# Performance work log

Hardware: AMD Instinct MI355X
Metric: run time of the kernel (lower is better)

Reference implementation:

```python
import jax, jax.numpy as jnp
import numpy as np

B, N = 16, 131072
C_MID, C_OUT = 128, 16


def setup_inputs() -> dict:
    key = jax.random.key(0)
    k1, k2, k3, k4 = jax.random.split(key, 4)
    # points in roughly [-0.5, 0.5] so cube indexing covers the grids
    x = jax.random.uniform(k1, (B, N, 3), dtype=jnp.float32) - 0.5
    W1 = jax.random.normal(k2, (C_MID, 3), dtype=jnp.float32) * 0.1
    b1 = jnp.zeros((C_MID,), jnp.float32)
    W2 = jax.random.normal(k3, (C_OUT, C_MID), dtype=jnp.float32) * 0.1
    b2 = jnp.zeros((C_OUT,), jnp.float32)
    # fixed per-batch permutations (deterministic stand-in for torch.randperm)
    perm = jnp.stack([jax.random.permutation(jax.random.fold_in(k4, i), N)
                      for i in range(B)]).astype(jnp.int32)
    return {"x": x, "W1": W1, "b1": b1, "W2": W2, "b2": b2, "perm": perm}


def point_to_cell(pts, feat, W, H, D):
    # pts float [B,N,3] already clamped to [0, dim-1]; cast like torch LongTensor
    idx = pts.astype(jnp.int32)
    flat = (idx[..., 0] * H + idx[..., 1]) * D + idx[..., 2]  # [B,N]
    Bb, Nn, C = feat.shape

    def scatter_one(fi, fe):
        grid = jnp.zeros((W * H * D, C), feat.dtype)
        return grid.at[fi].set(fe)

    cell = jax.vmap(scatter_one)(flat, feat)           # [B, WHD, C]
    return cell.transpose(0, 2, 1).reshape(Bb, C, W, H, D)


def reference(x, W1, b1, W2, b2, perm):
    # PointNetfeatLocal: 1x1 Conv1d stack == per-point MLP 3 -> 128 -> 16
    h = jnp.maximum(jnp.einsum('bnc,hc->bnh', x, W1) + b1, 0.0)
    feat = jnp.einsum('bnh,oh->bno', h, W2) + b2       # [B,N,16]
    # shuffle_points_feat: per-batch permutation gather
    xs = jnp.take_along_axis(x, perm[..., None], axis=1)
    fs = jnp.take_along_axis(feat, perm[..., None], axis=1)
    # batch_grid_pooling32 / 64
    cube32 = jnp.clip(xs * 32.0 + 16.5, 0.0, 31.0)
    cube64 = jnp.clip(xs * 64.0 + 32.5, 0.0, 63.0)
    feat_cell32 = point_to_cell(cube32, fs, 32, 32, 32)  # [B,16,32,32,32]
    feat_cell64 = point_to_cell(cube64, fs, 64, 64, 64)  # [B,16,64,64,64]
    return feat_cell32, feat_cell64
```

## Files before the change

### kernel.cpp

```cpp
#include <hip/hip_runtime.h>

namespace {
constexpr int kB = 16;
constexpr int kN = 131072;
constexpr int kNLog = 17;
constexpr int kCMid = 128;
constexpr int kCOut = 16;
constexpr int kCells32Log = 15;
constexpr int kCells64Log = 18;
constexpr int kCells32 = 1 << kCells32Log;
constexpr int kCells64 = 1 << kCells64Log;
constexpr long kOut32Elems = (long)kB * kCOut * kCells32;
constexpr int kP = 4;
}

__global__ __launch_bounds__(256) void pack_weights(
    const float* __restrict__ W1, const float* __restrict__ b1,
    const float* __restrict__ W2,
    float* __restrict__ W1p, float* __restrict__ W2t)
{
    const int t = threadIdx.x;
    for (int k = t; k < kCMid; k += 256) {
        W1p[k * 4 + 0] = W1[k * 3 + 0];
        W1p[k * 4 + 1] = W1[k * 3 + 1];
        W1p[k * 4 + 2] = W1[k * 3 + 2];
        W1p[k * 4 + 3] = b1[k];
    }
    for (int idx = t; idx < kCOut * kCMid; idx += 256) {
        const int c = idx >> 7;
        const int k = idx & 127;
        W2t[k * kCOut + c] = W2[idx];
    }
}

__global__ __launch_bounds__(256) void fused_mlp_scatter(
    const float* __restrict__ x,
    const int* __restrict__ perm,
    const float* __restrict__ W1p, const float* __restrict__ W2t,
    const float* __restrict__ b2,
    unsigned int* __restrict__ win32, unsigned int* __restrict__ win64,
    float* __restrict__ feat)
{
    const int t = threadIdx.x;
    const long base = (long)blockIdx.x * (256 * kP);

    float x0[kP], x1[kP], x2[kP];

    #pragma unroll
    for (int p = 0; p < kP; ++p) {
        const long gid = base + p * 256 + t;
        const int b = (int)(gid >> kNLog);
        const int i = (int)(gid & (kN - 1));
        const int j = perm[gid];
        const float* xp = x + ((long)b * kN + j) * 3;
        const float v0 = xp[0], v1 = xp[1], v2 = xp[2];
        x0[p] = v0; x1[p] = v1; x2[p] = v2;

        const int ix32 = (int)fminf(fmaxf(__fadd_rn(__fmul_rn(v0, 32.0f), 16.5f), 0.0f), 31.0f);
        const int iy32 = (int)fminf(fmaxf(__fadd_rn(__fmul_rn(v1, 32.0f), 16.5f), 0.0f), 31.0f);
        const int iz32 = (int)fminf(fmaxf(__fadd_rn(__fmul_rn(v2, 32.0f), 16.5f), 0.0f), 31.0f);
        const int ix64 = (int)fminf(fmaxf(__fadd_rn(__fmul_rn(v0, 64.0f), 32.5f), 0.0f), 63.0f);
        const int iy64 = (int)fminf(fmaxf(__fadd_rn(__fmul_rn(v1, 64.0f), 32.5f), 0.0f), 63.0f);
        const int iz64 = (int)fminf(fmaxf(__fadd_rn(__fmul_rn(v2, 64.0f), 32.5f), 0.0f), 63.0f);
        const unsigned int pri = (unsigned int)(i + 1);
        atomicMax(&win32[b * kCells32 + (ix32 * 32 + iy32) * 32 + iz32], pri);
        atomicMax(&win64[b * kCells64 + (ix64 * 64 + iy64) * 64 + iz64], pri);
    }

    float acc[kP][kCOut];
    #pragma unroll
    for (int p = 0; p < kP; ++p)
        #pragma unroll
        for (int c = 0; c < kCOut; ++c) acc[p][c] = 0.0f;

    const float4* __restrict__ w1v = (const float4*)W1p;
    const float4* __restrict__ w2v = (const float4*)W2t;

    #pragma unroll 4
    for (int k = 0; k < kCMid; ++k) {
        const float4 w1 = w1v[k];
        float h[kP];
        #pragma unroll
        for (int p = 0; p < kP; ++p)
            h[p] = fmaxf(fmaf(w1.x, x0[p], fmaf(w1.y, x1[p], fmaf(w1.z, x2[p], w1.w))), 0.0f);
        #pragma unroll
        for (int q = 0; q < 4; ++q) {
            const float4 w = w2v[k * 4 + q];
            #pragma unroll
            for (int p = 0; p < kP; ++p) {
                acc[p][4 * q + 0] = fmaf(w.x, h[p], acc[p][4 * q + 0]);
                acc[p][4 * q + 1] = fmaf(w.y, h[p], acc[p][4 * q + 1]);
                acc[p][4 * q + 2] = fmaf(w.z, h[p], acc[p][4 * q + 2]);
                acc[p][4 * q + 3] = fmaf(w.w, h[p], acc[p][4 * q + 3]);
            }
        }
    }

    const float4 bq0 = ((const float4*)b2)[0];
    const float4 bq1 = ((const float4*)b2)[1];
    const float4 bq2 = ((const float4*)b2)[2];
    const float4 bq3 = ((const float4*)b2)[3];

    #pragma unroll
    for (int p = 0; p < kP; ++p) {
        const long gid = base + p * 256 + t;
        float4* fp = (float4*)(feat + gid * kCOut);
        fp[0] = make_float4(acc[p][0]  + bq0.x, acc[p][1]  + bq0.y, acc[p][2]  + bq0.z, acc[p][3]  + bq0.w);
        fp[1] = make_float4(acc[p][4]  + bq1.x, acc[p][5]  + bq1.y, acc[p][6]  + bq1.z, acc[p][7]  + bq1.w);
        fp[2] = make_float4(acc[p][8]  + bq2.x, acc[p][9]  + bq2.y, acc[p][10] + bq2.z, acc[p][11] + bq2.w);
        fp[3] = make_float4(acc[p][12] + bq3.x, acc[p][13] + bq3.y, acc[p][14] + bq3.z, acc[p][15] + bq3.w);
    }
}

template <int CLOG, bool RECOMPUTE>
__global__ __launch_bounds__(256) void gather_cells(
    const unsigned int* __restrict__ win,
    const float* __restrict__ feat,
    const int* __restrict__ perm,
    const float* __restrict__ x,
    const float* __restrict__ W1p, const float* __restrict__ W2t,
    const float* __restrict__ b2,
    float* __restrict__ out)
{
    constexpr int cells = 1 << CLOG;
    const long gid = (long)blockIdx.x * 256 + threadIdx.x;
    const int b = (int)(gid >> CLOG);
    const int cell = (int)(gid & (cells - 1));
    const unsigned int w = win[gid];

    float v[kCOut];
    if (w == 0u) {
        #pragma unroll
        for (int c = 0; c < kCOut; ++c) v[c] = 0.0f;
    } else if (!RECOMPUTE) {
        const int i = (int)(w - 1u);
        const float4* fp = (const float4*)(feat + (((long)b << kNLog) + i) * kCOut);
        const float4 f0 = fp[0], f1 = fp[1], f2 = fp[2], f3 = fp[3];
        v[0] = f0.x; v[1] = f0.y; v[2]  = f0.z; v[3]  = f0.w;
        v[4] = f1.x; v[5] = f1.y; v[6]  = f1.z; v[7]  = f1.w;
        v[8] = f2.x; v[9] = f2.y; v[10] = f2.z; v[11] = f2.w;
        v[12] = f3.x; v[13] = f3.y; v[14] = f3.z; v[15] = f3.w;
    } else {
        const int i = (int)(w - 1u);
        const int j = perm[((long)b << kNLog) + i];
        const float* xp = x + ((long)b * kN + j) * 3;
        const float v0 = xp[0], v1 = xp[1], v2 = xp[2];
        #pragma unroll
        for (int c = 0; c < kCOut; ++c) v[c] = 0.0f;
        #pragma unroll 4
        for (int k = 0; k < kCMid; ++k) {
            const float4 w1 = ((const float4*)W1p)[k];
            const float h = fmaxf(fmaf(w1.x, v0, fmaf(w1.y, v1, fmaf(w1.z, v2, w1.w))), 0.0f);
            #pragma unroll
            for (int q = 0; q < 4; ++q) {
                const float4 wq = ((const float4*)W2t)[k * 4 + q];
                v[4 * q + 0] = fmaf(wq.x, h, v[4 * q + 0]);
                v[4 * q + 1] = fmaf(wq.y, h, v[4 * q + 1]);
                v[4 * q + 2] = fmaf(wq.z, h, v[4 * q + 2]);
                v[4 * q + 3] = fmaf(wq.w, h, v[4 * q + 3]);
            }
        }
        #pragma unroll
        for (int c = 0; c < kCOut; ++c) v[c] += b2[c];
    }

    float* op = out + (((long)b * kCOut) << CLOG) + cell;
    #pragma unroll
    for (int c = 0; c < kCOut; ++c) op[(long)c << CLOG] = v[c];
}

extern "C" void kernel_launch(void* const* d_in, const int* in_sizes, int n_in,
                              void* d_out, int out_size, void* d_ws, size_t ws_size,
                              hipStream_t stream)
{
    const float* x  = (const float*)d_in[0];
    const float* W1 = (const float*)d_in[1];
    const float* b1 = (const float*)d_in[2];
    const float* W2 = (const float*)d_in[3];
    const float* b2 = (const float*)d_in[4];
    const int* perm = (const int*)d_in[5];

    float* out32 = (float*)d_out;
    float* out64 = out32 + kOut32Elems;

    float* W1p = (float*)d_ws;
    float* W2t = W1p + kCMid * 4;
    unsigned int* win32 = (unsigned int*)((char*)d_ws + 16384);
    unsigned int* win64 = win32 + (size_t)kB * kCells32;
    const size_t winnerBytes = (size_t)kB * (kCells32 + kCells64) * sizeof(unsigned int);
    float* feat = (float*)((char*)win32 + winnerBytes);
    const size_t featBytes = (size_t)kB * kN * kCOut * sizeof(float);
    const bool storeFeat = ws_size >= 16384 + winnerBytes + featBytes;

    hipMemsetAsync(win32, 0, winnerBytes, stream);
    pack_weights<<<1, 256, 0, stream>>>(W1, b1, W2, W1p, W2t);

    const int nPtsBlocks = (int)(((long)kB * kN) / (256 * kP));
    const int n32Blocks  = (int)(((long)kB * kCells32) / 256);
    const int n64Blocks  = (int)(((long)kB * kCells64) / 256);
    dim3 blk(256);

    fused_mlp_scatter<<<nPtsBlocks, blk, 0, stream>>>(
        x, perm, W1p, W2t, b2, win32, win64, feat);

    if (storeFeat) {
        gather_cells<kCells32Log, false><<<n32Blocks, blk, 0, stream>>>(
            win32, feat, perm, x, W1p, W2t, b2, out32);
        gather_cells<kCells64Log, false><<<n64Blocks, blk, 0, stream>>>(
            win64, feat, perm, x, W1p, W2t, b2, out64);
    } else {
        gather_cells<kCells32Log, true><<<n32Blocks, blk, 0, stream>>>(
            win32, feat, perm, x, W1p, W2t, b2, out32);
        gather_cells<kCells64Log, true><<<n64Blocks, blk, 0, stream>>>(
            win64, feat, perm, x, W1p, W2t, b2, out64);
    }
}
```

Baseline: 320.6 us.

## Compute MLP only for winning points inside gather instead of materialising features

Drops the MLP from the scatter kernel, which now only records per-cell winning point indices. The gather kernels always recompute the 3→128→16 MLP for each occupied cell's winner, so the feature buffer is no longer written for all 2M points and read back. This removes the large feature write and gather read traffic and the MLP work for points that never win a cell. In exchange, occupied cells in both grids recompute the MLP, and points that win a cell in both grids are computed twice. Launch bounds of 4 blocks per SM are also added.

```diff
diff --git a/kernel.cpp b/kernel.cpp
--- a/kernel.cpp
+++ b/kernel.cpp
@@ -11,7 +11,6 @@
 constexpr int kCells32 = 1 << kCells32Log;
 constexpr int kCells64 = 1 << kCells64Log;
 constexpr long kOut32Elems = (long)kB * kCOut * kCells32;
-constexpr int kP = 4;
 }
 
 __global__ __launch_bounds__(256) void pack_weights(
@@ -33,89 +32,34 @@
     }
 }
 
-__global__ __launch_bounds__(256) void fused_mlp_scatter(
+__global__ __launch_bounds__(256, 4) void scatter_winners(
     const float* __restrict__ x,
     const int* __restrict__ perm,
-    const float* __restrict__ W1p, const float* __restrict__ W2t,
-    const float* __restrict__ b2,
-    unsigned int* __restrict__ win32, unsigned int* __restrict__ win64,
-    float* __restrict__ feat)
+    unsigned int* __restrict__ win32, unsigned int* __restrict__ win64)
 {
-    const int t = threadIdx.x;
-    const long base = (long)blockIdx.x * (256 * kP);
+    const long gid = (long)blockIdx.x * 256 + threadIdx.x;
+    const int b = (int)(gid >> kNLog);
+    const int i = (int)(gid & (kN - 1));
+    const int j = perm[gid];
 
-    float x0[kP], x1[kP], x2[kP];
+    const float* xp = x + ((long)b * kN + j) * 3;
+    const float v0 = xp[0], v1 = xp[1], v2 = xp[2];
 
-    #pragma unroll
-    for (int p = 0; p < kP; ++p) {
-        const long gid = base + p * 256 + t;
-        const int b = (int)(gid >> kNLog);
-        const int i = (int)(gid & (kN - 1));
-        const int j = perm[gid];
-        const float* xp = x + ((long)b * kN + j) * 3;
-        const float v0 = xp[0], v1 = xp[1], v2 = xp[2];
-        x0[p] = v0; x1[p] = v1; x2[p] = v2;
+    const int ix32 = (int)fminf(fmaxf(__fadd_rn(__fmul_rn(v0, 32.0f), 16.5f), 0.0f), 31.0f);
+    const int iy32 = (int)fminf(fmaxf(__fadd_rn(__fmul_rn(v1, 32.0f), 16.5f), 0.0f), 31.0f);
+    const int iz32 = (int)fminf(fmaxf(__fadd_rn(__fmul_rn(v2, 32.0f), 16.5f), 0.0f), 31.0f);
+    const int ix64 = (int)fminf(fmaxf(__fadd_rn(__fmul_rn(v0, 64.0f), 32.5f), 0.0f), 63.0f);
+    const int iy64 = (int)fminf(fmaxf(__fadd_rn(__fmul_rn(v1, 64.0f), 32.5f), 0.0f), 63.0f);
+    const int iz64 = (int)fminf(fmaxf(__fadd_rn(__fmul_rn(v2, 64.0f), 32.5f), 0.0f), 63.0f);
 
-        const int ix32 = (int)fminf(fmaxf(__fadd_rn(__fmul_rn(v0, 32.0f), 16.5f), 0.0f), 31.0f);
-        const int iy32 = (int)fminf(fmaxf(__fadd_rn(__fmul_rn(v1, 32.0f), 16.5f), 0.0f), 31.0f);
-        const int iz32 = (int)fminf(fmaxf(__fadd_rn(__fmul_rn(v2, 32.0f), 16.5f), 0.0f), 31.0f);
-        const int ix64 = (int)fminf(fmaxf(__fadd_rn(__fmul_rn(v0, 64.0f), 32.5f), 0.0f), 63.0f);
-        const int iy64 = (int)fminf(fmaxf(__fadd_rn(__fmul_rn(v1, 64.0f), 32.5f), 0.0f), 63.0f);
-        const int iz64 = (int)fminf(fmaxf(__fadd_rn(__fmul_rn(v2, 64.0f), 32.5f), 0.0f), 63.0f);
-        const unsigned int pri = (unsigned int)(i + 1);
-        atomicMax(&win32[b * kCells32 + (ix32 * 32 + iy32) * 32 + iz32], pri);
-        atomicMax(&win64[b * kCells64 + (ix64 * 64 + iy64) * 64 + iz64], pri);
-    }
-
-    float acc[kP][kCOut];
-    #pragma unroll
-    for (int p = 0; p < kP; ++p)
-        #pragma unroll
-        for (int c = 0; c < kCOut; ++c) acc[p][c] = 0.0f;
-
-    const float4* __restrict__ w1v = (const float4*)W1p;
-    const float4* __restrict__ w2v = (const float4*)W2t;
-
-    #pragma unroll 4
-    for (int k = 0; k < kCMid; ++k) {
-        const float4 w1 = w1v[k];
-        float h[kP];
-        #pragma unroll
-        for (int p = 0; p < kP; ++p)
-            h[p] = fmaxf(fmaf(w1.x, x0[p], fmaf(w1.y, x1[p], fmaf(w1.z, x2[p], w1.w))), 0.0f);
-        #pragma unroll
-        for (int q = 0; q < 4; ++q) {
-            const float4 w = w2v[k * 4 + q];
-            #pragma unroll
-            for (int p = 0; p < kP; ++p) {
-                acc[p][4 * q + 0] = fmaf(w.x, h[p], acc[p][4 * q + 0]);
-                acc[p][4 * q + 1] = fmaf(w.y, h[p], acc[p][4 * q + 1]);
-                acc[p][4 * q + 2] = fmaf(w.z, h[p], acc[p][4 * q + 2]);
-                acc[p][4 * q + 3] = fmaf(w.w, h[p], acc[p][4 * q + 3]);
-            }
-        }
-    }
-
-    const float4 bq0 = ((const float4*)b2)[0];
-    const float4 bq1 = ((const float4*)b2)[1];
-    const float4 bq2 = ((const float4*)b2)[2];
-    const float4 bq3 = ((const float4*)b2)[3];
-
-    #pragma unroll
-    for (int p = 0; p < kP; ++p) {
-        const long gid = base + p * 256 + t;
-        float4* fp = (float4*)(feat + gid * kCOut);
-        fp[0] = make_float4(acc[p][0]  + bq0.x, acc[p][1]  + bq0.y, acc[p][2]  + bq0.z, acc[p][3]  + bq0.w);
-        fp[1] = make_float4(acc[p][4]  + bq1.x, acc[p][5]  + bq1.y, acc[p][6]  + bq1.z, acc[p][7]  + bq1.w);
-        fp[2] = make_float4(acc[p][8]  + bq2.x, acc[p][9]  + bq2.y, acc[p][10] + bq2.z, acc[p][11] + bq2.w);
-        fp[3] = make_float4(acc[p][12] + bq3.x, acc[p][13] + bq3.y, acc[p][14] + bq3.z, acc[p][15] + bq3.w);
-    }
+    const unsigned int pri = (unsigned int)(i + 1);
+    atomicMax(&win32[b * kCells32 + (ix32 * 32 + iy32) * 32 + iz32], pri);
+    atomicMax(&win64[b * kCells64 + (ix64 * 64 + iy64) * 64 + iz64], pri);
 }
 
-template <int CLOG, bool RECOMPUTE>
-__global__ __launch_bounds__(256) void gather_cells(
+template <int CLOG>
+__global__ __launch_bounds__(256, 4) void gather_cells(
     const unsigned int* __restrict__ win,
-    const float* __restrict__ feat,
     const int* __restrict__ perm,
     const float* __restrict__ x,
     const float* __restrict__ W1p, const float* __restrict__ W2t,
@@ -129,31 +73,23 @@
     const unsigned int w = win[gid];
 
     float v[kCOut];
-    if (w == 0u) {
-        #pragma unroll
-        for (int c = 0; c < kCOut; ++c) v[c] = 0.0f;
-    } else if (!RECOMPUTE) {
-        const int i = (int)(w - 1u);
-        const float4* fp = (const float4*)(feat + (((long)b << kNLog) + i) * kCOut);
-        const float4 f0 = fp[0], f1 = fp[1], f2 = fp[2], f3 = fp[3];
-        v[0] = f0.x; v[1] = f0.y; v[2]  = f0.z; v[3]  = f0.w;
-        v[4] = f1.x; v[5] = f1.y; v[6]  = f1.z; v[7]  = f1.w;
-        v[8] = f2.x; v[9] = f2.y; v[10] = f2.z; v[11] = f2.w;
-        v[12] = f3.x; v[13] = f3.y; v[14] = f3.z; v[15] = f3.w;
-    } else {
+    #pragma unroll
+    for (int c = 0; c < kCOut; ++c) v[c] = 0.0f;
+
+    if (w != 0u) {
         const int i = (int)(w - 1u);
         const int j = perm[((long)b << kNLog) + i];
         const float* xp = x + ((long)b * kN + j) * 3;
         const float v0 = xp[0], v1 = xp[1], v2 = xp[2];
-        #pragma unroll
-        for (int c = 0; c < kCOut; ++c) v[c] = 0.0f;
+        const float4* __restrict__ w1v = (const float4*)W1p;
+        const float4* __restrict__ w2v = (const float4*)W2t;
         #pragma unroll 4
         for (int k = 0; k < kCMid; ++k) {
-            const float4 w1 = ((const float4*)W1p)[k];
+            const float4 w1 = w1v[k];
             const float h = fmaxf(fmaf(w1.x, v0, fmaf(w1.y, v1, fmaf(w1.z, v2, w1.w))), 0.0f);
             #pragma unroll
             for (int q = 0; q < 4; ++q) {
-                const float4 wq = ((const float4*)W2t)[k * 4 + q];
+                const float4 wq = w2v[k * 4 + q];
                 v[4 * q + 0] = fmaf(wq.x, h, v[4 * q + 0]);
                 v[4 * q + 1] = fmaf(wq.y, h, v[4 * q + 1]);
                 v[4 * q + 2] = fmaf(wq.z, h, v[4 * q + 2]);
@@ -188,30 +124,18 @@
     unsigned int* win32 = (unsigned int*)((char*)d_ws + 16384);
     unsigned int* win64 = win32 + (size_t)kB * kCells32;
     const size_t winnerBytes = (size_t)kB * (kCells32 + kCells64) * sizeof(unsigned int);
-    float* feat = (float*)((char*)win32 + winnerBytes);
-    const size_t featBytes = (size_t)kB * kN * kCOut * sizeof(float);
-    const bool storeFeat = ws_size >= 16384 + winnerBytes + featBytes;
 
     hipMemsetAsync(win32, 0, winnerBytes, stream);
     pack_weights<<<1, 256, 0, stream>>>(W1, b1, W2, W1p, W2t);
 
-    const int nPtsBlocks = (int)(((long)kB * kN) / (256 * kP));
+    const int nPtsBlocks = (int)(((long)kB * kN) / 256);
     const int n32Blocks  = (int)(((long)kB * kCells32) / 256);
     const int n64Blocks  = (int)(((long)kB * kCells64) / 256);
     dim3 blk(256);
 
-    fused_mlp_scatter<<<nPtsBlocks, blk, 0, stream>>>(
-        x, perm, W1p, W2t, b2, win32, win64, feat);
-
-    if (storeFeat) {
-        gather_cells<kCells32Log, false><<<n32Blocks, blk, 0, stream>>>(
-            win32, feat, perm, x, W1p, W2t, b2, out32);
-        gather_cells<kCells64Log, false><<<n64Blocks, blk, 0, stream>>>(
-            win64, feat, perm, x, W1p, W2t, b2, out64);
-    } else {
-        gather_cells<kCells32Log, true><<<n32Blocks, blk, 0, stream>>>(
-            win32, feat, perm, x, W1p, W2t, b2, out32);
-        gather_cells<kCells64Log, true><<<n64Blocks, blk, 0, stream>>>(
-            win64, feat, perm, x, W1p, W2t, b2, out64);
-    }
+    scatter_winners<<<nPtsBlocks, blk, 0, stream>>>(x, perm, win32, win64);
+    gather_cells<kCells32Log><<<n32Blocks, blk, 0, stream>>>(
+        win32, perm, x, W1p, W2t, b2, out32);
+    gather_cells<kCells64Log><<<n64Blocks, blk, 0, stream>>>(
+        win64, perm, x, W1p, W2t, b2, out64);
 }
```

Measured after the change: 422.2 us. 1.32x slower.
